# Kernel tuning notes

Hardware: AMD Instinct MI355X
Metric: run time of the kernel (lower is better)

## Reference

```python
import jax, jax.numpy as jnp
import numpy as np

B, C, H, W, D = 8, 192, 128, 128, 64


def setup_inputs() -> dict:
    key = jax.random.key(0)
    ks = jax.random.split(key, 9)
    s = 0.1
    return {
        'x': jax.random.normal(ks[0], (B, C, H, W), jnp.float32),
        'Wi': jax.random.normal(ks[1], (D, C), jnp.float32) * s,   # proj_in weight
        'bi': jax.random.normal(ks[2], (D,), jnp.float32) * s,
        'W_ih': jax.random.normal(ks[3], (3 * D, D), jnp.float32) * s,  # GRUCell weight_ih (r,z,n)
        'W_hh': jax.random.normal(ks[4], (3 * D, D), jnp.float32) * s,  # GRUCell weight_hh
        'b_ih': jax.random.normal(ks[5], (3 * D,), jnp.float32) * s,
        'b_hh': jax.random.normal(ks[6], (3 * D,), jnp.float32) * s,
        'Wo': jax.random.normal(ks[7], (C, D), jnp.float32) * s,   # proj_out weight
        'bo': jax.random.normal(ks[8], (C,), jnp.float32) * s,
    }


def _gru_scan(seq, W_ih, W_hh, b_ih, b_hh):
    # seq: (N, T, D). PyTorch GRUCell gate order: r, z, n.
    N, T, Dh = seq.shape[0], seq.shape[1], W_hh.shape[1]
    x_gates = jnp.einsum('ntd,gd->ntg', seq, W_ih) + b_ih  # (N, T, 3D), precomputed
    h0 = jnp.zeros((N, Dh), seq.dtype)

    def step(h, xg):
        hg = h @ W_hh.T + b_hh
        xr, xz, xn = jnp.split(xg, 3, axis=-1)
        hr, hz, hn = jnp.split(hg, 3, axis=-1)
        r = jax.nn.sigmoid(xr + hr)
        z = jax.nn.sigmoid(xz + hz)
        n = jnp.tanh(xn + r * hn)
        h_new = (1.0 - z) * n + z * h
        return h_new, h_new

    _, hs = jax.lax.scan(step, h0, jnp.swapaxes(x_gates, 0, 1))  # (T, N, D)
    return jnp.swapaxes(hs, 0, 1)  # (N, T, D)


def _scan_direction(x, Wi, bi, W_ih, W_hh, b_ih, b_hh, Wo, bo, transpose, reverse):
    b, c, h, w = x.shape
    # arrange to (B, A, T, C): scan along T (W for row scans, H for column scans)
    xs = jnp.transpose(x, (0, 3, 2, 1)) if transpose else jnp.transpose(x, (0, 2, 3, 1))
    if reverse:
        xs = xs[:, :, ::-1, :]
    A, T = xs.shape[1], xs.shape[2]
    seq = xs.reshape(b * A, T, c) @ Wi.T + bi              # proj_in -> (N, T, D)
    hs = _gru_scan(seq, W_ih, W_hh, b_ih, b_hh)            # (N, T, D)
    out = hs @ Wo.T + bo                                   # proj_out -> (N, T, C)
    out = out.reshape(b, A, T, c)
    if reverse:
        out = out[:, :, ::-1, :]
    return jnp.transpose(out, (0, 3, 2, 1)) if transpose else jnp.transpose(out, (0, 3, 1, 2))


def reference(x, Wi, bi, W_ih, W_hh, b_ih, b_hh, Wo, bo):
    p = (Wi, bi, W_ih, W_hh, b_ih, b_hh, Wo, bo)
    right = _scan_direction(x, *p, transpose=False, reverse=False)
    down = _scan_direction(x, *p, transpose=True, reverse=False)
    left = _scan_direction(x, *p, transpose=False, reverse=True)
    up = _scan_direction(x, *p, transpose=True, reverse=True)
    return (right + down + left + up) / 4.0
```

## Files before the change

kernel.cpp:

```cpp
#include <hip/hip_runtime.h>

#define Cn   192
#define Dn   64
#define G3   192
#define HWn  16384
#define NSp  131072L
#define Tn   128

typedef unsigned short u16;
typedef __attribute__((ext_vector_type(8))) short s8v;
typedef __attribute__((ext_vector_type(4))) float f4v;

__device__ __forceinline__ float bf2f(u16 u){
  union { unsigned int i; float f; } v; v.i = ((unsigned int)u) << 16; return v.f;
}
__device__ __forceinline__ u16 f2bf(float f){
  union { float f; unsigned int u; } v; v.f = f;
  return (u16)((v.u + 0x7FFFu + ((v.u >> 16) & 1u)) >> 16);
}
__device__ __forceinline__ s8v load8_f32_as_bf16(const float* __restrict__ p){
  s8v r;
  #pragma unroll
  for (int i = 0; i < 8; i++) r[i] = (short)f2bf(p[i]);
  return r;
}
__device__ __forceinline__ float ex2f(float x){
#if __has_builtin(__builtin_amdgcn_exp2f)
  return __builtin_amdgcn_exp2f(x);
#else
  float r; asm("v_exp_f32 %0, %1" : "=v"(r) : "v"(x)); return r;
#endif
}
__device__ __forceinline__ float rcpa(float x){
#if __has_builtin(__builtin_amdgcn_rcpf)
  return __builtin_amdgcn_rcpf(x);
#else
  float r; asm("v_rcp_f32 %0, %1" : "=v"(r) : "v"(x)); return r;
#endif
}

#define SC_RZ (-1.4426950408889634f)
#define SC_N  (-2.8853900817779268f)

__global__ __launch_bounds__(256) void k_wcomb(const float* __restrict__ Wi, const float* __restrict__ bi,
                                               const float* __restrict__ W_ih, const float* __restrict__ b_ih,
                                               const float* __restrict__ b_hh,
                                               u16* __restrict__ wcomb, float* __restrict__ bcomb){
  if (blockIdx.x < 144) {
    int idx = blockIdx.x * 256 + threadIdx.x;
    int g = idx / 192, c = idx - g * 192;
    float acc = 0.f;
    #pragma unroll 8
    for (int d = 0; d < 64; d++)
      acc += W_ih[g * 64 + d] * Wi[d * 192 + c];
    float sc = (g >= 128) ? SC_N : SC_RZ;
    wcomb[g * 192 + c] = f2bf(sc * acc);
  } else if (threadIdx.x < 192) {
    int g = threadIdx.x;
    float acc = b_ih[g];
    for (int d = 0; d < 64; d++)
      acc += W_ih[g * 64 + d] * bi[d];
    if (g < 128) acc += b_hh[g];
    float sc = (g >= 128) ? SC_N : SC_RZ;
    bcomb[g] = sc * acc;
  }
}

__global__ __launch_bounds__(256) void k_gates(const float* __restrict__ x, const u16* __restrict__ wcomb,
                                               const float* __restrict__ bcomb, u16* __restrict__ G){
  __shared__ u16 xT[64][200];
  const int tid = threadIdx.x;
  const int wave = tid >> 6, lane = tid & 63;
  const int col = lane & 15, kq = lane >> 4;
  const long s0 = (long)blockIdx.x * 64;
  const int b   = (int)(s0 >> 14);
  const int hw0 = (int)(s0 & 16383);

  s8v bfrag[3][6];
  #pragma unroll
  for (int j = 0; j < 3; j++) {
    int g = wave * 48 + j * 16 + col;
    #pragma unroll
    for (int kc = 0; kc < 6; kc++)
      bfrag[j][kc] = *(const s8v*)(wcomb + g * 192 + kc * 32 + kq * 8);
  }

  for (int idx = tid; idx < 192 * 16; idx += 256) {
    int c  = idx >> 4;
    int s4 = (idx & 15) * 4;
    float4 v = *(const float4*)(x + (long)(b * 192 + c) * HWn + hw0 + s4);
    xT[s4 + 0][c] = f2bf(v.x); xT[s4 + 1][c] = f2bf(v.y);
    xT[s4 + 2][c] = f2bf(v.z); xT[s4 + 3][c] = f2bf(v.w);
  }
  __syncthreads();

  f4v acc[4][3];
  #pragma unroll
  for (int m = 0; m < 4; m++)
    #pragma unroll
    for (int j = 0; j < 3; j++) acc[m][j] = (f4v){0.f, 0.f, 0.f, 0.f};

  #pragma unroll
  for (int kc = 0; kc < 6; kc++) {
    #pragma unroll
    for (int m = 0; m < 4; m++) {
      s8v a = *(const s8v*)(&xT[m * 16 + col][kc * 32 + kq * 8]);
      #pragma unroll
      for (int j = 0; j < 3; j++)
        acc[m][j] = __builtin_amdgcn_mfma_f32_16x16x32_bf16(a, bfrag[j][kc], acc[m][j], 0, 0, 0);
    }
  }

  #pragma unroll
  for (int j = 0; j < 3; j++) {
    int g = wave * 48 + j * 16 + col;
    float bias = bcomb[g];
    #pragma unroll
    for (int m = 0; m < 4; m++) {
      #pragma unroll
      for (int r = 0; r < 4; r++) {
        long srow = s0 + m * 16 + kq * 4 + r;
        G[srow * 192 + g] = f2bf(acc[m][j][r] + bias);
      }
    }
  }
}

__global__ __launch_bounds__(256) void k_scan(const u16* __restrict__ G, const float* __restrict__ W_hh,
                                              const float* __restrict__ b_hh, u16* __restrict__ Hall){
  __shared__ u16 ha[2][16][72];
  const int tid = threadIdx.x;
  const int w = tid >> 6, lane = tid & 63;
  const int col = lane & 15, kq = lane >> 4;
  const int dir  = blockIdx.x >> 6;
  const int sblk = blockIdx.x & 63;
  const int doff = 16 * w + 4 * kq;

  s8v afrag[3][2];
  #pragma unroll
  for (int g3 = 0; g3 < 3; g3++) {
    float sc = (g3 == 2) ? SC_N : SC_RZ;
    const float* wr = W_hh + (g3 * 64 + 16 * w + col) * 64;
    #pragma unroll
    for (int kc = 0; kc < 2; kc++) {
      s8v f;
      #pragma unroll
      for (int i = 0; i < 4; i++) f[i]     = (short)f2bf(sc * wr[kc * 32 +      4 * kq + i]);
      #pragma unroll
      for (int i = 0; i < 4; i++) f[4 + i] = (short)f2bf(sc * wr[kc * 32 + 16 + 4 * kq + i]);
      afrag[g3][kc] = f;
    }
  }
  f4v biasn;
  {
    const float* bb = b_hh + 128 + doff;
    biasn = (f4v){SC_N * bb[0], SC_N * bb[1], SC_N * bb[2], SC_N * bb[3]};
  }

  const int seq = sblk * 16 + col;
  const int b = seq >> 7, a = seq & 127;
  long base; int stride;
  if ((dir & 1) == 0) { base = ((long)(b * 128 + a)) * 128; stride = 1;   }
  else                { base = (long)b * 16384 + a;         stride = 128; }
  const int rev = dir >> 1;
  const long pd = rev ? -(long)stride : (long)stride;
  u16* __restrict__ Hs = Hall + (long)dir * (NSp * 64);
  const long pos0 = base + (long)(rev ? 127 : 0) * stride;
  const u16* gq = G  + pos0 * 192 + doff;
  u16*       hq = Hs + pos0 * 64  + doff;

  for (int i = tid; i < 2 * 16 * 72; i += 256) ((u16*)ha)[i] = 0;

  float hold[4] = {0.f, 0.f, 0.f, 0.f};

  uint2 xr0, xz0, xn0, xr1, xz1, xn1;
  xr0 = *(const uint2*)(gq); xz0 = *(const uint2*)(gq + 64); xn0 = *(const uint2*)(gq + 128);
  gq += pd * 192;
  xr1 = *(const uint2*)(gq); xz1 = *(const uint2*)(gq + 64); xn1 = *(const uint2*)(gq + 128);
  __syncthreads();

  int p = 0;
  for (int t = 0; t < 128; t++) {
    uint2 nxr, nxz, nxn;
    if (t < 126) {
      gq += pd * 192;
      nxr = *(const uint2*)(gq); nxz = *(const uint2*)(gq + 64); nxn = *(const uint2*)(gq + 128);
    }

    union BW { ushort4 q[2]; s8v v; } u0, u1;
    u0.q[0] = *(const ushort4*)(&ha[p][col][ 0 + 4 * kq]);
    u0.q[1] = *(const ushort4*)(&ha[p][col][16 + 4 * kq]);
    u1.q[0] = *(const ushort4*)(&ha[p][col][32 + 4 * kq]);
    u1.q[1] = *(const ushort4*)(&ha[p][col][48 + 4 * kq]);

    f4v acc0 = (f4v){0.f, 0.f, 0.f, 0.f};
    f4v acc1 = (f4v){0.f, 0.f, 0.f, 0.f};
    f4v acc2 = biasn;
    acc0 = __builtin_amdgcn_mfma_f32_16x16x32_bf16(afrag[0][0], u0.v, acc0, 0, 0, 0);
    acc1 = __builtin_amdgcn_mfma_f32_16x16x32_bf16(afrag[1][0], u0.v, acc1, 0, 0, 0);
    acc2 = __builtin_amdgcn_mfma_f32_16x16x32_bf16(afrag[2][0], u0.v, acc2, 0, 0, 0);
    acc0 = __builtin_amdgcn_mfma_f32_16x16x32_bf16(afrag[0][1], u1.v, acc0, 0, 0, 0);
    acc1 = __builtin_amdgcn_mfma_f32_16x16x32_bf16(afrag[1][1], u1.v, acc1, 0, 0, 0);
    acc2 = __builtin_amdgcn_mfma_f32_16x16x32_bf16(afrag[2][1], u1.v, acc2, 0, 0, 0);

    const u16* pxr = (const u16*)&xr0;
    const u16* pxz = (const u16*)&xz0;
    const u16* pxn = (const u16*)&xn0;
    float hh[4];
    #pragma unroll
    for (int r = 0; r < 4; r++) {
      float rr = rcpa(1.f + ex2f(bf2f(pxr[r]) + acc0[r]));
      float zz = rcpa(1.f + ex2f(bf2f(pxz[r]) + acc1[r]));
      float nn = 2.f * rcpa(1.f + ex2f(bf2f(pxn[r]) + rr * acc2[r])) - 1.f;
      float h  = nn + zz * (hold[r] - nn);
      hold[r] = h; hh[r] = h;
    }
    unsigned int w0, w1;
    asm("v_cvt_pk_bf16_f32 %0, %1, %2" : "=v"(w0) : "v"(hh[0]), "v"(hh[1]));
    asm("v_cvt_pk_bf16_f32 %0, %1, %2" : "=v"(w1) : "v"(hh[2]), "v"(hh[3]));
    uint2 wv; wv.x = w0; wv.y = w1;
    *(uint2*)(&ha[p ^ 1][col][doff]) = wv;
    *(uint2*)(hq) = wv;
    hq += pd * 64;

    xr0 = xr1; xz0 = xz1; xn0 = xn1;
    if (t < 126) { xr1 = nxr; xz1 = nxz; xn1 = nxn; }

    asm volatile("s_waitcnt lgkmcnt(0)" ::: "memory");
    __builtin_amdgcn_s_barrier();
    __builtin_amdgcn_sched_barrier(0);
    p ^= 1;
  }
}

__global__ __launch_bounds__(256) void k_out(const u16* __restrict__ Hall, const float* __restrict__ Wo,
                                             const float* __restrict__ bo, float* __restrict__ out){
  __shared__ u16 hs4[64][72];
  const int tid = threadIdx.x;
  const int wave = tid >> 6, lane = tid & 63;
  const int col = lane & 15, kq = lane >> 4;
  const long s0 = (long)blockIdx.x * 64;
  const int b   = (int)(s0 >> 14);
  const int hw0 = (int)(s0 & 16383);

  s8v bfrag[3][2]; f4v biasf[3];
  #pragma unroll
  for (int j = 0; j < 3; j++) {
    int g = wave * 48 + j * 16 + col;
    bfrag[j][0] = load8_f32_as_bf16(Wo + g * 64 + kq * 8);
    bfrag[j][1] = load8_f32_as_bf16(Wo + g * 64 + 32 + kq * 8);
    float bb = bo[g];
    biasf[j] = (f4v){bb, bb, bb, bb};
  }

  for (int idx = tid; idx < 64 * 16; idx += 256) {
    int sl = idx >> 4;
    int d4 = (idx & 15) * 4;
    long p = (s0 + sl) * 64 + d4;
    float a0 = 0.f, a1 = 0.f, a2 = 0.f, a3 = 0.f;
    #pragma unroll
    for (int dd = 0; dd < 4; dd++) {
      uint2 v = *(const uint2*)(Hall + dd * (NSp * 64) + p);
      u16* pv = (u16*)&v;
      a0 += bf2f(pv[0]); a1 += bf2f(pv[1]); a2 += bf2f(pv[2]); a3 += bf2f(pv[3]);
    }
    ushort4 o;
    o.x = f2bf(0.25f * a0); o.y = f2bf(0.25f * a1);
    o.z = f2bf(0.25f * a2); o.w = f2bf(0.25f * a3);
    *(ushort4*)(&hs4[sl][d4]) = o;
  }
  __syncthreads();

  f4v acc[4][3];
  #pragma unroll
  for (int m = 0; m < 4; m++)
    #pragma unroll
    for (int j = 0; j < 3; j++) acc[m][j] = biasf[j];

  #pragma unroll
  for (int kc = 0; kc < 2; kc++) {
    #pragma unroll
    for (int m = 0; m < 4; m++) {
      s8v a = *(const s8v*)(&hs4[m * 16 + col][kc * 32 + kq * 8]);
      #pragma unroll
      for (int j = 0; j < 3; j++)
        acc[m][j] = __builtin_amdgcn_mfma_f32_16x16x32_bf16(a, bfrag[j][kc], acc[m][j], 0, 0, 0);
    }
  }

  #pragma unroll
  for (int j = 0; j < 3; j++) {
    int g = wave * 48 + j * 16 + col;
    #pragma unroll
    for (int m = 0; m < 4; m++) {
      float4 v;
      v.x = acc[m][j][0]; v.y = acc[m][j][1];
      v.z = acc[m][j][2]; v.w = acc[m][j][3];
      long addr = ((long)(b * 192 + g) << 14) + hw0 + m * 16 + kq * 4;
      *(float4*)(out + addr) = v;
    }
  }
}

extern "C" void kernel_launch(void* const* d_in, const int* in_sizes, int n_in,
                              void* d_out, int out_size, void* d_ws, size_t ws_size,
                              hipStream_t stream){
  const float* x    = (const float*)d_in[0];
  const float* Wi   = (const float*)d_in[1];
  const float* bi   = (const float*)d_in[2];
  const float* W_ih = (const float*)d_in[3];
  const float* W_hh = (const float*)d_in[4];
  const float* b_ih = (const float*)d_in[5];
  const float* b_hh = (const float*)d_in[6];
  const float* Wo   = (const float*)d_in[7];
  const float* bo   = (const float*)d_in[8];

  char* ws = (char*)d_ws;
  u16*   wcomb = (u16*)(ws);
  float* bcomb = (float*)(ws + 73728);
  u16*   G     = (u16*)(ws + 74496);
  u16*   Hall  = (u16*)(ws + 50406144);

  k_wcomb<<<145,  256, 0, stream>>>(Wi, bi, W_ih, b_ih, b_hh, wcomb, bcomb);
  k_gates<<<2048, 256, 0, stream>>>(x, wcomb, bcomb, G);
  k_scan <<<256,  256, 0, stream>>>(G, W_hh, b_hh, Hall);
  k_out  <<<2048, 256, 0, stream>>>(Hall, Wo, bo, (float*)d_out);
}
```

Before: 306.1 us.

## Interleave gate layout in G for vectorized stores and packed scan loads

The gates kernel swaps MFMA operand roles so each lane holds four consecutive gate outputs. It writes G in an interleaved layout where each thread's r, z and n quads sit contiguously (12 elements), using packed bf16 conversions instead of scattered 2-byte stores. The scan kernel reads this layout with adjacent loads and uses single 16-byte LDS reads for the hidden-state fragments, after reordering the W_hh fragment columns to match. The output kernel widens the four-direction Hall reads to 16-byte loads. These changes aim to cut uncoalesced store traffic in the gates kernel and per-step load instructions in the scan, at the cost of a layout that both kernels must agree on.

```diff
diff --git a/kernel.cpp b/kernel.cpp
--- a/kernel.cpp
+++ b/kernel.cpp
@@ -38,9 +38,13 @@
   float r; asm("v_rcp_f32 %0, %1" : "=v"(r) : "v"(x)); return r;
 #endif
 }
+__device__ __forceinline__ unsigned int pk2bf(float a, float b){
+  unsigned int r; asm("v_cvt_pk_bf16_f32 %0, %1, %2" : "=v"(r) : "v"(a), "v"(b)); return r;
+}
 
 #define SC_RZ (-1.4426950408889634f)
 #define SC_N  (-2.8853900817779268f)
+
 
 __global__ __launch_bounds__(256) void k_wcomb(const float* __restrict__ Wi, const float* __restrict__ bi,
                                                const float* __restrict__ W_ih, const float* __restrict__ b_ih,
@@ -75,14 +79,17 @@
   const long s0 = (long)blockIdx.x * 64;
   const int b   = (int)(s0 >> 14);
   const int hw0 = (int)(s0 & 16383);
-
-  s8v bfrag[3][6];
-  #pragma unroll
-  for (int j = 0; j < 3; j++) {
-    int g = wave * 48 + j * 16 + col;
+  const int dq  = 4 * wave + kq;
+
+  s8v afrag[3][6];
+  f4v biasv[3];
+  #pragma unroll
+  for (int g3 = 0; g3 < 3; g3++) {
+    int g = g3 * 64 + 16 * wave + col;
     #pragma unroll
     for (int kc = 0; kc < 6; kc++)
-      bfrag[j][kc] = *(const s8v*)(wcomb + g * 192 + kc * 32 + kq * 8);
+      afrag[g3][kc] = *(const s8v*)(wcomb + g * 192 + kc * 32 + kq * 8);
+    biasv[g3] = *(const f4v*)(bcomb + g3 * 64 + 16 * wave + 4 * kq);
   }
 
   for (int idx = tid; idx < 192 * 16; idx += 256) {
@@ -96,32 +103,30 @@
 
   f4v acc[4][3];
   #pragma unroll
-  for (int m = 0; m < 4; m++)
-    #pragma unroll
-    for (int j = 0; j < 3; j++) acc[m][j] = (f4v){0.f, 0.f, 0.f, 0.f};
+  for (int nt = 0; nt < 4; nt++)
+    #pragma unroll
+    for (int g3 = 0; g3 < 3; g3++) acc[nt][g3] = biasv[g3];
 
   #pragma unroll
   for (int kc = 0; kc < 6; kc++) {
     #pragma unroll
-    for (int m = 0; m < 4; m++) {
-      s8v a = *(const s8v*)(&xT[m * 16 + col][kc * 32 + kq * 8]);
-      #pragma unroll
-      for (int j = 0; j < 3; j++)
-        acc[m][j] = __builtin_amdgcn_mfma_f32_16x16x32_bf16(a, bfrag[j][kc], acc[m][j], 0, 0, 0);
-    }
-  }
-
-  #pragma unroll
-  for (int j = 0; j < 3; j++) {
-    int g = wave * 48 + j * 16 + col;
-    float bias = bcomb[g];
-    #pragma unroll
-    for (int m = 0; m < 4; m++) {
-      #pragma unroll
-      for (int r = 0; r < 4; r++) {
-        long srow = s0 + m * 16 + kq * 4 + r;
-        G[srow * 192 + g] = f2bf(acc[m][j][r] + bias);
-      }
+    for (int nt = 0; nt < 4; nt++) {
+      s8v bx = *(const s8v*)(&xT[nt * 16 + col][kc * 32 + kq * 8]);
+      #pragma unroll
+      for (int g3 = 0; g3 < 3; g3++)
+        acc[nt][g3] = __builtin_amdgcn_mfma_f32_16x16x32_bf16(afrag[g3][kc], bx, acc[nt][g3], 0, 0, 0);
+    }
+  }
+
+  #pragma unroll
+  for (int nt = 0; nt < 4; nt++) {
+    long sRow = (s0 + nt * 16 + col) * 192 + dq * 12;
+    #pragma unroll
+    for (int g3 = 0; g3 < 3; g3++) {
+      uint2 wv;
+      wv.x = pk2bf(acc[nt][g3][0], acc[nt][g3][1]);
+      wv.y = pk2bf(acc[nt][g3][2], acc[nt][g3][3]);
+      *(uint2*)(G + sRow + g3 * 4) = wv;
     }
   }
 }
@@ -135,6 +140,7 @@
   const int dir  = blockIdx.x >> 6;
   const int sblk = blockIdx.x & 63;
   const int doff = 16 * w + 4 * kq;
+  const int dq   = 4 * w + kq;
 
   s8v afrag[3][2];
   #pragma unroll
@@ -145,9 +151,7 @@
     for (int kc = 0; kc < 2; kc++) {
       s8v f;
       #pragma unroll
-      for (int i = 0; i < 4; i++) f[i]     = (short)f2bf(sc * wr[kc * 32 +      4 * kq + i]);
-      #pragma unroll
-      for (int i = 0; i < 4; i++) f[4 + i] = (short)f2bf(sc * wr[kc * 32 + 16 + 4 * kq + i]);
+      for (int i = 0; i < 8; i++) f[i] = (short)f2bf(sc * wr[kc * 32 + kq * 8 + i]);
       afrag[g3][kc] = f;
     }
   }
@@ -166,7 +170,7 @@
   const long pd = rev ? -(long)stride : (long)stride;
   u16* __restrict__ Hs = Hall + (long)dir * (NSp * 64);
   const long pos0 = base + (long)(rev ? 127 : 0) * stride;
-  const u16* gq = G  + pos0 * 192 + doff;
+  const u16* gq = G  + pos0 * 192 + dq * 12;
   u16*       hq = Hs + pos0 * 64  + doff;
 
   for (int i = tid; i < 2 * 16 * 72; i += 256) ((u16*)ha)[i] = 0;
@@ -174,9 +178,9 @@
   float hold[4] = {0.f, 0.f, 0.f, 0.f};
 
   uint2 xr0, xz0, xn0, xr1, xz1, xn1;
-  xr0 = *(const uint2*)(gq); xz0 = *(const uint2*)(gq + 64); xn0 = *(const uint2*)(gq + 128);
+  xr0 = *(const uint2*)(gq); xz0 = *(const uint2*)(gq + 4); xn0 = *(const uint2*)(gq + 8);
   gq += pd * 192;
-  xr1 = *(const uint2*)(gq); xz1 = *(const uint2*)(gq + 64); xn1 = *(const uint2*)(gq + 128);
+  xr1 = *(const uint2*)(gq); xz1 = *(const uint2*)(gq + 4); xn1 = *(const uint2*)(gq + 8);
   __syncthreads();
 
   int p = 0;
@@ -184,24 +188,21 @@
     uint2 nxr, nxz, nxn;
     if (t < 126) {
       gq += pd * 192;
-      nxr = *(const uint2*)(gq); nxz = *(const uint2*)(gq + 64); nxn = *(const uint2*)(gq + 128);
-    }
-
-    union BW { ushort4 q[2]; s8v v; } u0, u1;
-    u0.q[0] = *(const ushort4*)(&ha[p][col][ 0 + 4 * kq]);
-    u0.q[1] = *(const ushort4*)(&ha[p][col][16 + 4 * kq]);
-    u1.q[0] = *(const ushort4*)(&ha[p][col][32 + 4 * kq]);
-    u1.q[1] = *(const ushort4*)(&ha[p][col][48 + 4 * kq]);
+      nxr = *(const uint2*)(gq); nxz = *(const uint2*)(gq + 4); nxn = *(const uint2*)(gq + 8);
+    }
+
+    s8v u0 = *(const s8v*)(&ha[p][col][kq * 8]);
+    s8v u1 = *(const s8v*)(&ha[p][col][32 + kq * 8]);
 
     f4v acc0 = (f4v){0.f, 0.f, 0.f, 0.f};
     f4v acc1 = (f4v){0.f, 0.f, 0.f, 0.f};
     f4v acc2 = biasn;
-    acc0 = __builtin_amdgcn_mfma_f32_16x16x32_bf16(afrag[0][0], u0.v, acc0, 0, 0, 0);
-    acc1 = __builtin_amdgcn_mfma_f32_16x16x32_bf16(afrag[1][0], u0.v, acc1, 0, 0, 0);
-    acc2 = __builtin_amdgcn_mfma_f32_16x16x32_bf16(afrag[2][0], u0.v, acc2, 0, 0, 0);
-    acc0 = __builtin_amdgcn_mfma_f32_16x16x32_bf16(afrag[0][1], u1.v, acc0, 0, 0, 0);
-    acc1 = __builtin_amdgcn_mfma_f32_16x16x32_bf16(afrag[1][1], u1.v, acc1, 0, 0, 0);
-    acc2 = __builtin_amdgcn_mfma_f32_16x16x32_bf16(afrag[2][1], u1.v, acc2, 0, 0, 0);
+    acc0 = __builtin_amdgcn_mfma_f32_16x16x32_bf16(afrag[0][0], u0, acc0, 0, 0, 0);
+    acc1 = __builtin_amdgcn_mfma_f32_16x16x32_bf16(afrag[1][0], u0, acc1, 0, 0, 0);
+    acc2 = __builtin_amdgcn_mfma_f32_16x16x32_bf16(afrag[2][0], u0, acc2, 0, 0, 0);
+    acc0 = __builtin_amdgcn_mfma_f32_16x16x32_bf16(afrag[0][1], u1, acc0, 0, 0, 0);
+    acc1 = __builtin_amdgcn_mfma_f32_16x16x32_bf16(afrag[1][1], u1, acc1, 0, 0, 0);
+    acc2 = __builtin_amdgcn_mfma_f32_16x16x32_bf16(afrag[2][1], u1, acc2, 0, 0, 0);
 
     const u16* pxr = (const u16*)&xr0;
     const u16* pxz = (const u16*)&xz0;
@@ -215,10 +216,9 @@
       float h  = nn + zz * (hold[r] - nn);
       hold[r] = h; hh[r] = h;
     }
-    unsigned int w0, w1;
-    asm("v_cvt_pk_bf16_f32 %0, %1, %2" : "=v"(w0) : "v"(hh[0]), "v"(hh[1]));
-    asm("v_cvt_pk_bf16_f32 %0, %1, %2" : "=v"(w1) : "v"(hh[2]), "v"(hh[3]));
-    uint2 wv; wv.x = w0; wv.y = w1;
+    uint2 wv;
+    wv.x = pk2bf(hh[0], hh[1]);
+    wv.y = pk2bf(hh[2], hh[3]);
     *(uint2*)(&ha[p ^ 1][col][doff]) = wv;
     *(uint2*)(hq) = wv;
     hq += pd * 64;
@@ -253,21 +253,31 @@
     biasf[j] = (f4v){bb, bb, bb, bb};
   }
 
-  for (int idx = tid; idx < 64 * 16; idx += 256) {
-    int sl = idx >> 4;
-    int d4 = (idx & 15) * 4;
-    long p = (s0 + sl) * 64 + d4;
-    float a0 = 0.f, a1 = 0.f, a2 = 0.f, a3 = 0.f;
-    #pragma unroll
-    for (int dd = 0; dd < 4; dd++) {
-      uint2 v = *(const uint2*)(Hall + dd * (NSp * 64) + p);
-      u16* pv = (u16*)&v;
-      a0 += bf2f(pv[0]); a1 += bf2f(pv[1]); a2 += bf2f(pv[2]); a3 += bf2f(pv[3]);
-    }
-    ushort4 o;
-    o.x = f2bf(0.25f * a0); o.y = f2bf(0.25f * a1);
-    o.z = f2bf(0.25f * a2); o.w = f2bf(0.25f * a3);
-    *(ushort4*)(&hs4[sl][d4]) = o;
+  for (int idx = tid; idx < 64 * 8; idx += 256) {
+    int sl = idx >> 3;
+    int d8 = (idx & 7) * 8;
+    long p = (s0 + sl) * 64 + d8;
+    float s[8];
+    {
+      uint4 v = *(const uint4*)(Hall + p);
+      const u16* pv = (const u16*)&v;
+      #pragma unroll
+      for (int i = 0; i < 8; i++) s[i] = bf2f(pv[i]);
+    }
+    #pragma unroll
+    for (int dd = 1; dd < 4; dd++) {
+      uint4 v = *(const uint4*)(Hall + dd * (NSp * 64) + p);
+      const u16* pv = (const u16*)&v;
+      #pragma unroll
+      for (int i = 0; i < 8; i++) s[i] += bf2f(pv[i]);
+    }
+    uint2 w0, w1;
+    w0.x = pk2bf(0.25f * s[0], 0.25f * s[1]);
+    w0.y = pk2bf(0.25f * s[2], 0.25f * s[3]);
+    w1.x = pk2bf(0.25f * s[4], 0.25f * s[5]);
+    w1.y = pk2bf(0.25f * s[6], 0.25f * s[7]);
+    *(uint2*)(&hs4[sl][d8]) = w0;
+    *(uint2*)(&hs4[sl][d8 + 4]) = w1;
   }
   __syncthreads();
 
```

Measured after the change: 297.6 us. 1.03x faster.
